# Performance work log

Measured on AMD Instinct MI355X. Metric: run time of the kernel, lower is better.

## Reference

```python
import jax, jax.numpy as jnp
import numpy as np


def setup_inputs() -> dict:
    key = jax.random.key(0)
    ks = jax.random.split(key, 7)
    B, S1, S2, D, H, P = 4, 2048, 2048, 512, 8, 64
    return {
        "q": jax.random.normal(ks[0], (B, S1, D), dtype=jnp.float32),
        "k": jax.random.normal(ks[1], (B, S2, D), dtype=jnp.float32),
        "v": jax.random.normal(ks[2], (B, S2, D), dtype=jnp.float32),
        "Wq": jax.random.normal(ks[3], (H, D, P), dtype=jnp.float32),
        "Wk": jax.random.normal(ks[4], (H, D, P), dtype=jnp.float32),
        "Wv": jax.random.normal(ks[5], (H, D, P), dtype=jnp.float32),
        "Wo": jax.random.normal(ks[6], (H * P, D), dtype=jnp.float32),
    }


def reference(q, k, v, Wq, Wk, Wv, Wo):
    # Per-head projections: [B,S,D] x [H,D,P] -> [B,H,S,P]
    qh = jnp.einsum("bsd,hdp->bhsp", q, Wq)
    kh = jnp.einsum("btd,hdp->bhtp", k, Wk)
    vh = jnp.einsum("btd,hdp->bhtp", v, Wv)
    P = Wq.shape[-1]
    scale = 1.0 / np.sqrt(P).astype(np.float32)
    # Naive attention with full [B,H,S1,S2] scores, as in the original
    scores = jnp.einsum("bhsp,bhtp->bhst", qh, kh) * scale
    att = jax.nn.softmax(scores, axis=-1)
    out = jnp.einsum("bhst,bhtp->bhsp", att, vh)
    # Concat heads along feature dim: [B,S1,H*P]
    B, H, S1, _ = out.shape
    out = out.transpose(0, 2, 1, 3).reshape(B, S1, H * P)
    # Output projection (dropout is identity in eval / p=0)
    return out @ Wo
```

## Files before the change

kernel.cpp:

```cpp
#include <hip/hip_runtime.h>
#include <hip/hip_bf16.h>

typedef __attribute__((ext_vector_type(8))) short bf16x8;
typedef __attribute__((ext_vector_type(4))) float f32x4;

#define MFMA __builtin_amdgcn_mfma_f32_16x16x32_bf16

__device__ __forceinline__ unsigned short f2bf(float f) {
    unsigned int u = __builtin_bit_cast(unsigned int, f);
    u += 0x7fffu + ((u >> 16) & 1u);
    return (unsigned short)(u >> 16);
}
__device__ __forceinline__ float bf2f(unsigned short h) {
    unsigned int u = ((unsigned int)h) << 16;
    return __builtin_bit_cast(float, u);
}

__global__ __launch_bounds__(256) void prep_w(const float* __restrict__ W,
                                              unsigned short* __restrict__ hi,
                                              unsigned short* __restrict__ lo,
                                              float scale, int hpd) {
    int tid = blockIdx.x * 256 + threadIdx.x;
    int col = tid >> 9, d = tid & 511;
    float x;
    if (hpd) x = W[(size_t)(col >> 6) * (512 * 64) + (size_t)d * 64 + (col & 63)];
    else     x = W[(size_t)d * 512 + col];
    x *= scale;
    unsigned short h = f2bf(x);
    hi[tid] = h;
    if (lo) lo[tid] = f2bf(x - bf2f(h));
}

__global__ __launch_bounds__(256) void proj_kernel(
    const float* __restrict__ X,
    const unsigned short* __restrict__ Wh,
    const unsigned short* __restrict__ Wl,
    unsigned short* __restrict__ Oh,
    unsigned short* __restrict__ Ol,
    int mode)
{
    const int lane = threadIdx.x & 63;
    const int wave = threadIdx.x >> 6;
    const int lr = lane & 15, lg = lane >> 4;
    const int rb = blockIdx.x >> 3;
    const int cb = blockIdx.x & 7;
    const int row0 = rb * 128 + wave * 32;
    const int col0 = cb * 64;

    f32x4 acc[2][4];
#pragma unroll
    for (int m = 0; m < 2; ++m)
#pragma unroll
        for (int n = 0; n < 4; ++n) acc[m][n] = {0.f, 0.f, 0.f, 0.f};

    for (int ks = 0; ks < 16; ++ks) {
        const int d0 = ks * 32 + lg * 8;
        bf16x8 ah[2], al[2];
#pragma unroll
        for (int m = 0; m < 2; ++m) {
            const float* px = X + (size_t)(row0 + m * 16 + lr) * 512 + d0;
            f32x4 x0 = *reinterpret_cast<const f32x4*>(px);
            f32x4 x1 = *reinterpret_cast<const f32x4*>(px + 4);
#pragma unroll
            for (int j = 0; j < 4; ++j) {
                unsigned short h0 = f2bf(x0[j]);
                unsigned short h1 = f2bf(x1[j]);
                ah[m][j]     = (short)h0;
                ah[m][j + 4] = (short)h1;
                al[m][j]     = (short)f2bf(x0[j] - bf2f(h0));
                al[m][j + 4] = (short)f2bf(x1[j] - bf2f(h1));
            }
        }
#pragma unroll
        for (int n = 0; n < 4; ++n) {
            size_t woff = (size_t)(col0 + n * 16 + lr) * 512 + d0;
            bf16x8 bh = *reinterpret_cast<const bf16x8*>(Wh + woff);
            bf16x8 bl = *reinterpret_cast<const bf16x8*>(Wl + woff);
#pragma unroll
            for (int m = 0; m < 2; ++m) {
                f32x4 a = acc[m][n];
                a = MFMA(ah[m], bh, a, 0, 0, 0);
                a = MFMA(al[m], bh, a, 0, 0, 0);
                a = MFMA(ah[m], bl, a, 0, 0, 0);
                acc[m][n] = a;
            }
        }
    }

#pragma unroll
    for (int m = 0; m < 2; ++m)
#pragma unroll
        for (int n = 0; n < 4; ++n)
#pragma unroll
            for (int r = 0; r < 4; ++r) {
                int grow = row0 + m * 16 + lg * 4 + r;
                int col  = col0 + n * 16 + lr;
                int b = grow >> 11, s = grow & 2047;
                int h = col >> 6,  p = col & 63;
                float v = acc[m][n][r];
                if (mode == 0) {
                    size_t o = ((size_t)(b * 8 + h) * 2048 + s) * 64 + p;
                    unsigned short hv = f2bf(v);
                    Oh[o] = hv;
                    Ol[o] = f2bf(v - bf2f(hv));
                } else {
                    size_t o = ((size_t)(b * 8 + h) * 64 + p) * 2048 + s;
                    Oh[o] = f2bf(v);
                }
            }
}

__global__ __launch_bounds__(256) void attn_kernel(
    const unsigned short* __restrict__ Qh, const unsigned short* __restrict__ Ql,
    const unsigned short* __restrict__ Kh, const unsigned short* __restrict__ Kl,
    const unsigned short* __restrict__ VT,
    unsigned short* __restrict__ Att)
{
    __shared__ __align__(16) unsigned char plds[4 * 32 * 144];
    const int lane = threadIdx.x & 63;
    const int wave = threadIdx.x >> 6;
    const int lr = lane & 15, lg = lane >> 4;
    const int bh = blockIdx.x >> 4;
    const int qt = blockIdx.x & 15;
    const int q0 = qt * 128 + wave * 32;
    unsigned char* pl = plds + wave * (32 * 144);

    bf16x8 qfh[2][2], qfl[2][2];
#pragma unroll
    for (int m = 0; m < 2; ++m)
#pragma unroll
        for (int ks = 0; ks < 2; ++ks) {
            size_t off = ((size_t)bh * 2048 + q0 + m * 16 + lr) * 64 + ks * 32 + lg * 8;
            qfh[m][ks] = *reinterpret_cast<const bf16x8*>(Qh + off);
            qfl[m][ks] = *reinterpret_cast<const bf16x8*>(Ql + off);
        }

    f32x4 oacc[2][4];
    f32x4 mrun[2], lrun[2];
#pragma unroll
    for (int m = 0; m < 2; ++m) {
        mrun[m] = {-1e30f, -1e30f, -1e30f, -1e30f};
        lrun[m] = {0.f, 0.f, 0.f, 0.f};
#pragma unroll
        for (int n = 0; n < 4; ++n) oacc[m][n] = {0.f, 0.f, 0.f, 0.f};
    }

    const float LOG2E = 1.4426950408889634f;

    for (int kt = 0; kt < 32; ++kt) {
        f32x4 sc[2][4];
#pragma unroll
        for (int n = 0; n < 4; ++n) {
            size_t koff = ((size_t)bh * 2048 + kt * 64 + n * 16 + lr) * 64 + lg * 8;
            bf16x8 kh0 = *reinterpret_cast<const bf16x8*>(Kh + koff);
            bf16x8 kh1 = *reinterpret_cast<const bf16x8*>(Kh + koff + 32);
            bf16x8 kl0 = *reinterpret_cast<const bf16x8*>(Kl + koff);
            bf16x8 kl1 = *reinterpret_cast<const bf16x8*>(Kl + koff + 32);
#pragma unroll
            for (int m = 0; m < 2; ++m) {
                f32x4 a = {0.f, 0.f, 0.f, 0.f};
                a = MFMA(qfh[m][0], kh0, a, 0, 0, 0);
                a = MFMA(qfh[m][1], kh1, a, 0, 0, 0);
                a = MFMA(qfl[m][0], kh0, a, 0, 0, 0);
                a = MFMA(qfl[m][1], kh1, a, 0, 0, 0);
                a = MFMA(qfh[m][0], kl0, a, 0, 0, 0);
                a = MFMA(qfh[m][1], kl1, a, 0, 0, 0);
                sc[m][n] = a;
            }
        }

#pragma unroll
        for (int m = 0; m < 2; ++m) {
            f32x4 tmax;
#pragma unroll
            for (int r = 0; r < 4; ++r)
                tmax[r] = fmaxf(fmaxf(sc[m][0][r], sc[m][1][r]),
                                fmaxf(sc[m][2][r], sc[m][3][r]));
#pragma unroll
            for (int msk = 1; msk < 16; msk <<= 1)
#pragma unroll
                for (int r = 0; r < 4; ++r)
                    tmax[r] = fmaxf(tmax[r], __shfl_xor(tmax[r], msk));

            f32x4 mnew, scale, rsum;
#pragma unroll
            for (int r = 0; r < 4; ++r) {
                mnew[r]  = fmaxf(mrun[m][r], tmax[r]);
                scale[r] = exp2f((mrun[m][r] - mnew[r]) * LOG2E);
                rsum[r]  = 0.f;
            }
#pragma unroll
            for (int n = 0; n < 4; ++n)
#pragma unroll
                for (int r = 0; r < 4; ++r) {
                    float p = exp2f((sc[m][n][r] - mnew[r]) * LOG2E);
                    sc[m][n][r] = p;
                    rsum[r] += p;
                }
#pragma unroll
            for (int msk = 1; msk < 16; msk <<= 1)
#pragma unroll
                for (int r = 0; r < 4; ++r)
                    rsum[r] += __shfl_xor(rsum[r], msk);
#pragma unroll
            for (int r = 0; r < 4; ++r)
                lrun[m][r] = lrun[m][r] * scale[r] + rsum[r];
            mrun[m] = mnew;
#pragma unroll
            for (int n = 0; n < 4; ++n)
#pragma unroll
                for (int r = 0; r < 4; ++r)
                    oacc[m][n][r] *= scale[r];
        }

#pragma unroll
        for (int m = 0; m < 2; ++m)
#pragma unroll
            for (int n = 0; n < 4; ++n)
#pragma unroll
                for (int r = 0; r < 4; ++r) {
                    int s = m * 16 + lg * 4 + r;
                    int t = n * 16 + lr;
                    int addr = s * 144 + ((2 * t) ^ ((s & 7) << 4));
                    *reinterpret_cast<unsigned short*>(pl + addr) = f2bf(sc[m][n][r]);
                }

        bf16x8 pa[2][2];
#pragma unroll
        for (int m = 0; m < 2; ++m)
#pragma unroll
            for (int ks = 0; ks < 2; ++ks) {
                int s = m * 16 + lr;
                int t0 = ks * 32 + lg * 8;
                int addr = s * 144 + ((2 * t0) ^ ((s & 7) << 4));
                pa[m][ks] = *reinterpret_cast<const bf16x8*>(pl + addr);
            }

#pragma unroll
        for (int n = 0; n < 4; ++n) {
            size_t voff = ((size_t)bh * 64 + n * 16 + lr) * 2048 + kt * 64 + lg * 8;
            bf16x8 vb0 = *reinterpret_cast<const bf16x8*>(VT + voff);
            bf16x8 vb1 = *reinterpret_cast<const bf16x8*>(VT + voff + 32);
#pragma unroll
            for (int m = 0; m < 2; ++m) {
                f32x4 a = oacc[m][n];
                a = MFMA(pa[m][0], vb0, a, 0, 0, 0);
                a = MFMA(pa[m][1], vb1, a, 0, 0, 0);
                oacc[m][n] = a;
            }
        }
    }

    const int b = bh >> 3, h = bh & 7;
#pragma unroll
    for (int m = 0; m < 2; ++m) {
        f32x4 inv;
#pragma unroll
        for (int r = 0; r < 4; ++r) inv[r] = 1.0f / lrun[m][r];
#pragma unroll
        for (int n = 0; n < 4; ++n)
#pragma unroll
            for (int r = 0; r < 4; ++r) {
                int s = q0 + m * 16 + lg * 4 + r;
                int p = n * 16 + lr;
                Att[((size_t)b * 2048 + s) * 512 + h * 64 + p] =
                    f2bf(oacc[m][n][r] * inv[r]);
            }
    }
}

__global__ __launch_bounds__(256) void outproj_kernel(
    const unsigned short* __restrict__ A,
    const unsigned short* __restrict__ WT,
    float* __restrict__ Out)
{
    const int lane = threadIdx.x & 63;
    const int wave = threadIdx.x >> 6;
    const int lr = lane & 15, lg = lane >> 4;
    const int rb = blockIdx.x >> 3;
    const int cb = blockIdx.x & 7;
    const int row0 = rb * 128 + wave * 32;
    const int col0 = cb * 64;

    f32x4 acc[2][4];
#pragma unroll
    for (int m = 0; m < 2; ++m)
#pragma unroll
        for (int n = 0; n < 4; ++n) acc[m][n] = {0.f, 0.f, 0.f, 0.f};

    for (int ks = 0; ks < 16; ++ks) {
        const int k0 = ks * 32 + lg * 8;
        bf16x8 af[2];
#pragma unroll
        for (int m = 0; m < 2; ++m)
            af[m] = *reinterpret_cast<const bf16x8*>(A + (size_t)(row0 + m * 16 + lr) * 512 + k0);
#pragma unroll
        for (int n = 0; n < 4; ++n) {
            bf16x8 bf = *reinterpret_cast<const bf16x8*>(WT + (size_t)(col0 + n * 16 + lr) * 512 + k0);
#pragma unroll
            for (int m = 0; m < 2; ++m)
                acc[m][n] = MFMA(af[m], bf, acc[m][n], 0, 0, 0);
        }
    }

#pragma unroll
    for (int m = 0; m < 2; ++m)
#pragma unroll
        for (int n = 0; n < 4; ++n)
#pragma unroll
            for (int r = 0; r < 4; ++r)
                Out[(size_t)(row0 + m * 16 + lg * 4 + r) * 512 + col0 + n * 16 + lr] =
                    acc[m][n][r];
}

extern "C" void kernel_launch(void* const* d_in, const int* in_sizes, int n_in,
                              void* d_out, int out_size, void* d_ws, size_t ws_size,
                              hipStream_t stream) {
    (void)in_sizes; (void)n_in; (void)out_size; (void)ws_size;
    const float* q  = (const float*)d_in[0];
    const float* k  = (const float*)d_in[1];
    const float* v  = (const float*)d_in[2];
    const float* Wq = (const float*)d_in[3];
    const float* Wk = (const float*)d_in[4];
    const float* Wv = (const float*)d_in[5];
    const float* Wo = (const float*)d_in[6];
    float* out = (float*)d_out;

    size_t off = 0;
    auto take = [&](size_t bytes) -> void* {
        void* p = (char*)d_ws + off;
        off += (bytes + 255) & ~(size_t)255;
        return p;
    };
    const size_t WSZ = 512 * 512 * sizeof(unsigned short);
    const size_t BSZ = (size_t)32 * 2048 * 64 * sizeof(unsigned short);

    unsigned short* WqTh = (unsigned short*)take(WSZ);
    unsigned short* WqTl = (unsigned short*)take(WSZ);
    unsigned short* WkTh = (unsigned short*)take(WSZ);
    unsigned short* WkTl = (unsigned short*)take(WSZ);
    unsigned short* WvTh = (unsigned short*)take(WSZ);
    unsigned short* WvTl = (unsigned short*)take(WSZ);
    unsigned short* WoT  = (unsigned short*)take(WSZ);
    unsigned short* Qh   = (unsigned short*)take(BSZ);
    unsigned short* Ql   = (unsigned short*)take(BSZ);
    unsigned short* Kh   = (unsigned short*)take(BSZ);
    unsigned short* Kl   = (unsigned short*)take(BSZ);
    unsigned short* VT   = (unsigned short*)take(BSZ);
    unsigned short* Att  = (unsigned short*)take(BSZ);

    prep_w<<<1024, 256, 0, stream>>>(Wq, WqTh, WqTl, 0.125f, 1);
    prep_w<<<1024, 256, 0, stream>>>(Wk, WkTh, WkTl, 1.0f, 1);
    prep_w<<<1024, 256, 0, stream>>>(Wv, WvTh, WvTl, 1.0f, 1);
    prep_w<<<1024, 256, 0, stream>>>(Wo, WoT, nullptr, 1.0f, 0);

    proj_kernel<<<512, 256, 0, stream>>>(q, WqTh, WqTl, Qh, Ql, 0);
    proj_kernel<<<512, 256, 0, stream>>>(k, WkTh, WkTl, Kh, Kl, 0);
    proj_kernel<<<512, 256, 0, stream>>>(v, WvTh, WvTl, VT, nullptr, 1);

    attn_kernel<<<512, 256, 0, stream>>>(Qh, Ql, Kh, Kl, VT, Att);

    outproj_kernel<<<512, 256, 0, stream>>>(Att, WoT, out);
}
```

Baseline: 481.3 us.

## Fold softmax row-sum into PV MFMA, lazy rescale, smaller tiles, XCD-aware block mapping

Result: slower. 649.9 us (+35.0%).

```diff
diff --git a/kernel.cpp b/kernel.cpp
--- a/kernel.cpp
+++ b/kernel.cpp
@@ -31,6 +31,15 @@
     if (lo) lo[tid] = f2bf(x - bf2f(h));
 }
 
+__global__ __launch_bounds__(256) void vt_init(unsigned short* __restrict__ VT) {
+    int tid = blockIdx.x * 256 + threadIdx.x;
+    int t = tid & 2047;
+    int rr = (tid >> 11) & 15;
+    int bh = tid >> 15;
+    VT[((size_t)bh * 80 + 64 + rr) * 2048 + t] =
+        (rr == 0) ? (unsigned short)0x3F80 : (unsigned short)0;
+}
+
 __global__ __launch_bounds__(256) void proj_kernel(
     const float* __restrict__ X,
     const unsigned short* __restrict__ Wh,
@@ -42,8 +51,11 @@
     const int lane = threadIdx.x & 63;
     const int wave = threadIdx.x >> 6;
     const int lr = lane & 15, lg = lane >> 4;
-    const int rb = blockIdx.x >> 3;
-    const int cb = blockIdx.x & 7;
+    const int blk = blockIdx.x;
+    const int xcd = blk & 7;
+    const int loc = blk >> 3;
+    const int rb = xcd * 8 + (loc >> 3);
+    const int cb = loc & 7;
     const int row0 = rb * 128 + wave * 32;
     const int col0 = cb * 64;
 
@@ -90,65 +102,70 @@
 #pragma unroll
     for (int m = 0; m < 2; ++m)
 #pragma unroll
-        for (int n = 0; n < 4; ++n)
-#pragma unroll
-            for (int r = 0; r < 4; ++r) {
-                int grow = row0 + m * 16 + lg * 4 + r;
-                int col  = col0 + n * 16 + lr;
-                int b = grow >> 11, s = grow & 2047;
-                int h = col >> 6,  p = col & 63;
-                float v = acc[m][n][r];
-                if (mode == 0) {
+        for (int n = 0; n < 4; ++n) {
+            int col = col0 + n * 16 + lr;
+            int h = col >> 6, p = col & 63;
+            if (mode == 0) {
+#pragma unroll
+                for (int r = 0; r < 4; ++r) {
+                    int grow = row0 + m * 16 + lg * 4 + r;
+                    int b = grow >> 11, s = grow & 2047;
+                    float v = acc[m][n][r];
                     size_t o = ((size_t)(b * 8 + h) * 2048 + s) * 64 + p;
                     unsigned short hv = f2bf(v);
                     Oh[o] = hv;
                     Ol[o] = f2bf(v - bf2f(hv));
-                } else {
-                    size_t o = ((size_t)(b * 8 + h) * 64 + p) * 2048 + s;
-                    Oh[o] = f2bf(v);
                 }
-            }
-}
-
-__global__ __launch_bounds__(256) void attn_kernel(
+            } else {
+                int grow0 = row0 + m * 16 + lg * 4;
+                int b = grow0 >> 11, s0 = grow0 & 2047;
+                ushort4 pk;
+                pk.x = f2bf(acc[m][n][0]);
+                pk.y = f2bf(acc[m][n][1]);
+                pk.z = f2bf(acc[m][n][2]);
+                pk.w = f2bf(acc[m][n][3]);
+                *reinterpret_cast<ushort4*>(
+                    Oh + ((size_t)(b * 8 + h) * 80 + p) * 2048 + s0) = pk;
+            }
+        }
+}
+
+__global__ __launch_bounds__(256, 4) void attn_kernel(
     const unsigned short* __restrict__ Qh, const unsigned short* __restrict__ Ql,
     const unsigned short* __restrict__ Kh, const unsigned short* __restrict__ Kl,
     const unsigned short* __restrict__ VT,
     unsigned short* __restrict__ Att)
 {
-    __shared__ __align__(16) unsigned char plds[4 * 32 * 144];
+    __shared__ __align__(16) unsigned char plds[4 * 16 * 144];
     const int lane = threadIdx.x & 63;
     const int wave = threadIdx.x >> 6;
     const int lr = lane & 15, lg = lane >> 4;
-    const int bh = blockIdx.x >> 4;
-    const int qt = blockIdx.x & 15;
-    const int q0 = qt * 128 + wave * 32;
-    unsigned char* pl = plds + wave * (32 * 144);
-
-    bf16x8 qfh[2][2], qfl[2][2];
-#pragma unroll
-    for (int m = 0; m < 2; ++m)
-#pragma unroll
-        for (int ks = 0; ks < 2; ++ks) {
-            size_t off = ((size_t)bh * 2048 + q0 + m * 16 + lr) * 64 + ks * 32 + lg * 8;
-            qfh[m][ks] = *reinterpret_cast<const bf16x8*>(Qh + off);
-            qfl[m][ks] = *reinterpret_cast<const bf16x8*>(Ql + off);
-        }
-
-    f32x4 oacc[2][4];
-    f32x4 mrun[2], lrun[2];
-#pragma unroll
-    for (int m = 0; m < 2; ++m) {
-        mrun[m] = {-1e30f, -1e30f, -1e30f, -1e30f};
-        lrun[m] = {0.f, 0.f, 0.f, 0.f};
-#pragma unroll
-        for (int n = 0; n < 4; ++n) oacc[m][n] = {0.f, 0.f, 0.f, 0.f};
-    }
+    const int blk = blockIdx.x;
+    const int xcd = blk & 7;
+    const int loc = blk >> 3;
+    const int bh  = xcd * 4 + (loc >> 5);
+    const int qt  = loc & 31;
+    const int q0 = qt * 64 + wave * 16;
+    unsigned char* pl = plds + wave * (16 * 144);
+
+    bf16x8 qfh[2], qfl[2];
+#pragma unroll
+    for (int ks = 0; ks < 2; ++ks) {
+        size_t off = ((size_t)bh * 2048 + q0 + lr) * 64 + ks * 32 + lg * 8;
+        qfh[ks] = *reinterpret_cast<const bf16x8*>(Qh + off);
+        qfl[ks] = *reinterpret_cast<const bf16x8*>(Ql + off);
+    }
+
+    f32x4 oacc[5];
+    f32x4 mrun;
+#pragma unroll
+    for (int n = 0; n < 5; ++n) oacc[n] = {0.f, 0.f, 0.f, 0.f};
+    mrun = {-1e30f, -1e30f, -1e30f, -1e30f};
 
     const float LOG2E = 1.4426950408889634f;
 
     for (int kt = 0; kt < 32; ++kt) {
-        f32x4 sc[2][4];
+        f32x4 sc[4];
 #pragma unroll
         for (int n = 0; n < 4; ++n) {
             size_t koff = ((size_t)bh * 2048 + kt * 64 + n * 16 + lr) * 64 + lg * 8;
@@ -156,117 +173,94 @@
             bf16x8 kh1 = *reinterpret_cast<const bf16x8*>(Kh + koff + 32);
             bf16x8 kl0 = *reinterpret_cast<const bf16x8*>(Kl + koff);
             bf16x8 kl1 = *reinterpret_cast<const bf16x8*>(Kl + koff + 32);
-#pragma unroll
-            for (int m = 0; m < 2; ++m) {
-                f32x4 a = {0.f, 0.f, 0.f, 0.f};
-                a = MFMA(qfh[m][0], kh0, a, 0, 0, 0);
-                a = MFMA(qfh[m][1], kh1, a, 0, 0, 0);
-                a = MFMA(qfl[m][0], kh0, a, 0, 0, 0);
-                a = MFMA(qfl[m][1], kh1, a, 0, 0, 0);
-                a = MFMA(qfh[m][0], kl0, a, 0, 0, 0);
-                a = MFMA(qfh[m][1], kl1, a, 0, 0, 0);
-                sc[m][n] = a;
-            }
-        }
-
-#pragma unroll
-        for (int m = 0; m < 2; ++m) {
-            f32x4 tmax;
+            f32x4 a = {0.f, 0.f, 0.f, 0.f};
+            a = MFMA(qfh[0], kh0, a, 0, 0, 0);
+            a = MFMA(qfh[1], kh1, a, 0, 0, 0);
+            a = MFMA(qfl[0], kh0, a, 0, 0, 0);
+            a = MFMA(qfl[1], kh1, a, 0, 0, 0);
+            a = MFMA(qfh[0], kl0, a, 0, 0, 0);
+            a = MFMA(qfh[1], kl1, a, 0, 0, 0);
+            sc[n] = a;
+        }
+
+        f32x4 tmax;
+#pragma unroll
+        for (int r = 0; r < 4; ++r)
+            tmax[r] = fmaxf(fmaxf(sc[0][r], sc[1][r]), fmaxf(sc[2][r], sc[3][r]));
+#pragma unroll
+        for (int msk = 1; msk < 16; msk <<= 1)
 #pragma unroll
             for (int r = 0; r < 4; ++r)
-                tmax[r] = fmaxf(fmaxf(sc[m][0][r], sc[m][1][r]),
-                                fmaxf(sc[m][2][r], sc[m][3][r]));
-#pragma unroll
-            for (int msk = 1; msk < 16; msk <<= 1)
-#pragma unroll
-                for (int r = 0; r < 4; ++r)
-                    tmax[r] = fmaxf(tmax[r], __shfl_xor(tmax[r], msk));
-
-            f32x4 mnew, scale, rsum;
+                tmax[r] = fmaxf(tmax[r], __shfl_xor(tmax[r], msk));
+
+        int need = 0;
+#pragma unroll
+        for (int r = 0; r < 4; ++r) need |= (tmax[r] > mrun[r] + 8.0f) ? 1 : 0;
+        if (__any(need)) {
+            f32x4 scale;
 #pragma unroll
             for (int r = 0; r < 4; ++r) {
-                mnew[r]  = fmaxf(mrun[m][r], tmax[r]);
-                scale[r] = exp2f((mrun[m][r] - mnew[r]) * LOG2E);
-                rsum[r]  = 0.f;
-            }
-#pragma unroll
-            for (int n = 0; n < 4; ++n)
-#pragma unroll
-                for (int r = 0; r < 4; ++r) {
-                    float p = exp2f((sc[m][n][r] - mnew[r]) * LOG2E);
-                    sc[m][n][r] = p;
-                    rsum[r] += p;
-                }
-#pragma unroll
-            for (int msk = 1; msk < 16; msk <<= 1)
-#pragma unroll
-                for (int r = 0; r < 4; ++r)
-                    rsum[r] += __shfl_xor(rsum[r], msk);
-#pragma unroll
-            for (int r = 0; r < 4; ++r)
-                lrun[m][r] = lrun[m][r] * scale[r] + rsum[r];
-            mrun[m] = mnew;
-#pragma unroll
-            for (int n = 0; n < 4; ++n)
-#pragma unroll
-                for (int r = 0; r < 4; ++r)
-                    oacc[m][n][r] *= scale[r];
-        }
-
-#pragma unroll
-        for (int m = 0; m < 2; ++m)
-#pragma unroll
-            for (int n = 0; n < 4; ++n)
-#pragma unroll
-                for (int r = 0; r < 4; ++r) {
-                    int s = m * 16 + lg * 4 + r;
-                    int t = n * 16 + lr;
-                    int addr = s * 144 + ((2 * t) ^ ((s & 7) << 4));
-                    *reinterpret_cast<unsigned short*>(pl + addr) = f2bf(sc[m][n][r]);
-                }
-
-        bf16x8 pa[2][2];
-#pragma unroll
-        for (int m = 0; m < 2; ++m)
-#pragma unroll
-            for (int ks = 0; ks < 2; ++ks) {
-                int s = m * 16 + lr;
-                int t0 = ks * 32 + lg * 8;
-                int addr = s * 144 + ((2 * t0) ^ ((s & 7) << 4));
-                pa[m][ks] = *reinterpret_cast<const bf16x8*>(pl + addr);
-            }
-
-#pragma unroll
-        for (int n = 0; n < 4; ++n) {
-            size_t voff = ((size_t)bh * 64 + n * 16 + lr) * 2048 + kt * 64 + lg * 8;
+                float mnew = fmaxf(mrun[r], tmax[r]);
+                scale[r] = exp2f((mrun[r] - mnew) * LOG2E);
+                mrun[r] = mnew;
+            }
+#pragma unroll
+            for (int n = 0; n < 5; ++n)
+#pragma unroll
+                for (int r = 0; r < 4; ++r) oacc[n][r] *= scale[r];
+        }
+
+        f32x4 mb;
+#pragma unroll
+        for (int r = 0; r < 4; ++r) mb[r] = mrun[r] * LOG2E;
+#pragma unroll
+        for (int n = 0; n < 4; ++n)
+#pragma unroll
+            for (int r = 0; r < 4; ++r) {
+                float p = exp2f(sc[n][r] * LOG2E - mb[r]);
+                int s = lg * 4 + r;
+                int t = n * 16 + lr;
+                int addr = s * 144 + ((2 * t) ^ ((s & 7) << 4));
+                *reinterpret_cast<unsigned short*>(pl + addr) = f2bf(p);
+            }
+
+        bf16x8 pa[2];
+#pragma unroll
+        for (int ks = 0; ks < 2; ++ks) {
+            int s = lr;
+            int t0 = ks * 32 + lg * 8;
+            int addr = s * 144 + ((2 * t0) ^ ((s & 7) << 4));
+            pa[ks] = *reinterpret_cast<const bf16x8*>(pl + addr);
+        }
+
+#pragma unroll
+        for (int n = 0; n < 5; ++n) {
+            size_t voff = ((size_t)bh * 80 + n * 16 + lr) * 2048 + kt * 64 + lg * 8;
             bf16x8 vb0 = *reinterpret_cast<const bf16x8*>(VT + voff);
             bf16x8 vb1 = *reinterpret_cast<const bf16x8*>(VT + voff + 32);
-#pragma unroll
-            for (int m = 0; m < 2; ++m) {
-                f32x4 a = oacc[m][n];
-                a = MFMA(pa[m][0], vb0, a, 0, 0, 0);
-                a = MFMA(pa[m][1], vb1, a, 0, 0, 0);
-                oacc[m][n] = a;
-            }
+            f32x4 a = oacc[n];
+            a = MFMA(pa[0], vb0, a, 0, 0, 0);
+            a = MFMA(pa[1], vb1, a, 0, 0, 0);
+            oacc[n] = a;
         }
     }
 
     const int b = bh >> 3, h = bh & 7;
-#pragma unroll
-    for (int m = 0; m < 2; ++m) {
-        f32x4 inv;
-#pragma unroll
-        for (int r = 0; r < 4; ++r) inv[r] = 1.0f / lrun[m][r];
-#pragma unroll
-        for (int n = 0; n < 4; ++n)
-#pragma unroll
-            for (int r = 0; r < 4; ++r) {
-                int s = q0 + m * 16 + lg * 4 + r;
-                int p = n * 16 + lr;
-                Att[((size_t)b * 2048 + s) * 512 + h * 64 + p] =
-                    f2bf(oacc[m][n][r] * inv[r]);
-            }
-    }
+    f32x4 inv;
+#pragma unroll
+    for (int r = 0; r < 4; ++r) {
+        float denom = __shfl(oacc[4][r], (lane & 48));
+        inv[r] = 1.0f / denom;
+    }
+#pragma unroll
+    for (int n = 0; n < 4; ++n)
+#pragma unroll
+        for (int r = 0; r < 4; ++r) {
+            int s = q0 + lg * 4 + r;
+            int p = n * 16 + lr;
+            Att[((size_t)b * 2048 + s) * 512 + h * 64 + p] =
+                f2bf(oacc[n][r] * inv[r]);
+        }
 }
 
 __global__ __launch_bounds__(256) void outproj_kernel(
@@ -277,8 +271,11 @@
     const int lane = threadIdx.x & 63;
     const int wave = threadIdx.x >> 6;
     const int lr = lane & 15, lg = lane >> 4;
-    const int rb = blockIdx.x >> 3;
-    const int cb = blockIdx.x & 7;
+    const int blk = blockIdx.x;
+    const int xcd = blk & 7;
+    const int loc = blk >> 3;
+    const int rb = xcd * 8 + (loc >> 3);
+    const int cb = loc & 7;
     const int row0 = rb * 128 + wave * 32;
     const int col0 = cb * 64;
 
@@ -332,8 +329,9 @@
         off += (bytes + 255) & ~(size_t)255;
         return p;
     };
-    const size_t WSZ = 512 * 512 * sizeof(unsigned short);
-    const size_t BSZ = (size_t)32 * 2048 * 64 * sizeof(unsigned short);
+    const size_t WSZ  = 512 * 512 * sizeof(unsigned short);
+    const size_t BSZ  = (size_t)32 * 2048 * 64 * sizeof(unsigned short);
+    const size_t VTSZ = (size_t)32 * 80 * 2048 * sizeof(unsigned short);
 
     unsigned short* WqTh = (unsigned short*)take(WSZ);
     unsigned short* WqTl = (unsigned short*)take(WSZ);
@@ -346,19 +344,20 @@
     unsigned short* Ql   = (unsigned short*)take(BSZ);
     unsigned short* Kh   = (unsigned short*)take(BSZ);
     unsigned short* Kl   = (unsigned short*)take(BSZ);
-    unsigned short* VT   = (unsigned short*)take(BSZ);
+    unsigned short* VT   = (unsigned short*)take(VTSZ);
     unsigned short* Att  = (unsigned short*)take(BSZ);
 
     prep_w<<<1024, 256, 0, stream>>>(Wq, WqTh, WqTl, 0.125f, 1);
     prep_w<<<1024, 256, 0, stream>>>(Wk, WkTh, WkTl, 1.0f, 1);
     prep_w<<<1024, 256, 0, stream>>>(Wv, WvTh, WvTl, 1.0f, 1);
     prep_w<<<1024, 256, 0, stream>>>(Wo, WoT, nullptr, 1.0f, 0);
+    vt_init<<<4096, 256, 0, stream>>>(VT);
 
     proj_kernel<<<512, 256, 0, stream>>>(q, WqTh, WqTl, Qh, Ql, 0);
     proj_kernel<<<512, 256, 0, stream>>>(k, WkTh, WkTl, Kh, Kl, 0);
     proj_kernel<<<512, 256, 0, stream>>>(v, WvTh, WvTl, VT, nullptr, 1);
 
-    attn_kernel<<<512, 256, 0, stream>>>(Qh, Ql, Kh, Kl, VT, Att);
+    attn_kernel<<<1024, 256, 0, stream>>>(Qh, Ql, Kh, Kl, VT, Att);
 
     outproj_kernel<<<512, 256, 0, stream>>>(Att, WoT, out);
 }
```
